# Optimization experiments

Hardware: AMD Instinct MI355X
Metric: run time of the kernel (lower is better)

The kernel has to match this reference:

```python
import jax, jax.numpy as jnp
import numpy as np

B, N, F, W = 8, 2048, 128, 64


def setup_inputs() -> dict:
    key = jax.random.key(0)
    k1, k2, k3, k4 = jax.random.split(key, 4)
    x = jax.random.normal(k1, (B, N, F), dtype=jnp.float32)
    adj = jnp.ones((B, N, N), dtype=bool)  # accepted by forward but unused
    w_key = jax.random.normal(k2, (F, W), dtype=jnp.float32) * 0.1
    w_value = jax.random.normal(k3, (F, F), dtype=jnp.float32) * 0.1
    w_query = jax.random.normal(k4, (F, W), dtype=jnp.float32) * 0.1
    return {"x": x, "adj": adj, "w_key": w_key, "w_value": w_value, "w_query": w_query}


def reference(x, adj, w_key, w_value, w_query):
    # keys/queries: [B, N, W]; values: [B, N, F]
    keys = x @ w_key
    querys = x @ w_query
    values = x @ w_value
    # per-batch softmax(Q K^T) over last dim -> [B, N, N]
    scores = jax.nn.softmax(jnp.einsum('bnw,bmw->bnm', querys, keys), axis=-1)
    # original broadcast-multiply-sum is exactly scores @ values
    out = jnp.einsum('bnm,bmf->bnf', scores, values)
    return out
```

## Files before the change

kernel.cpp:

```cpp
#include <hip/hip_runtime.h>
#include <hip/hip_bf16.h>
#include <math.h>

constexpr int B = 8;
constexpr int N = 2048;
constexpr int F = 128;
constexpr int W = 64;

constexpr int TQ = 64;
constexpr int TK = 64;
constexpr int KSPLIT = 2;
constexpr int TILES_PER_SPLIT = (N / TK) / KSPLIT;

typedef short bf16x8 __attribute__((ext_vector_type(8)));
typedef float f32x4  __attribute__((ext_vector_type(4)));

__device__ inline ushort f2bf(float f) {
  union { float f; uint u; } v; v.f = f;
  uint u = v.u;
  return (ushort)((u + 0x7FFFu + ((u >> 16) & 1u)) >> 16);
}
__device__ inline float bf2f(ushort h) {
  union { uint u; float f; } v; v.u = ((uint)h) << 16;
  return v.f;
}
__device__ inline void splitbf(float f, ushort& hi, ushort& lo) {
  ushort h = f2bf(f);
  hi = h;
  lo = f2bf(f - bf2f(h));
}

__global__ __launch_bounds__(256) void prep_w(
    const float* __restrict__ wq, const float* __restrict__ wk,
    const float* __restrict__ wv, ushort* __restrict__ wth,
    ushort* __restrict__ wtl) {
  int gid = blockIdx.x * 256 + threadIdx.x;
  int n = gid >> 4;
  int k0 = (gid & 15) * 8;
  ushort th[8], tl[8];
#pragma unroll
  for (int j = 0; j < 8; ++j) {
    int k = k0 + j;
    float val = (n < 64)  ? wq[k * W + n]
              : (n < 128) ? wk[k * W + (n - 64)]
                          : wv[k * F + (n - 128)];
    splitbf(val, th[j], tl[j]);
  }
  *(uint4*)&wth[n * 128 + k0] = *(uint4*)th;
  *(uint4*)&wtl[n * 128 + k0] = *(uint4*)tl;
}

__global__ __launch_bounds__(256) void proj_kernel(
    const float* __restrict__ x,
    const ushort* __restrict__ wth, const ushort* __restrict__ wtl,
    ushort* __restrict__ q_h, ushort* __restrict__ q_l,
    ushort* __restrict__ k_h, ushort* __restrict__ k_l,
    ushort* __restrict__ vt_ws) {
  const int tid  = threadIdx.x;
  const int wid  = tid >> 6;
  const int lane = tid & 63;
  const int lg = lane >> 4, li = lane & 15;
  const int rb   = blockIdx.x & 255;
  const int half = blockIdx.x >> 8;
  const int brow0 = rb * 64;
  const int b    = brow0 / N;
  const int nloc = brow0 % N;

  bf16x8 xh[4], xl[4];
  const float* xrow = x + (size_t)(brow0 + wid * 16 + li) * F;
#pragma unroll
  for (int kk = 0; kk < 4; ++kk) {
    float4 a = *(const float4*)&xrow[kk * 32 + lg * 8];
    float4 c = *(const float4*)&xrow[kk * 32 + lg * 8 + 4];
    float vals[8] = {a.x, a.y, a.z, a.w, c.x, c.y, c.z, c.w};
    ushort hh[8], ll[8];
#pragma unroll
    for (int j = 0; j < 8; ++j) splitbf(vals[j], hh[j], ll[j]);
    xh[kk] = *(bf16x8*)hh;
    xl[kk] = *(bf16x8*)ll;
  }

  f32x4 zero = {0.f, 0.f, 0.f, 0.f};
  f32x4 acc[8];
#pragma unroll
  for (int t = 0; t < 8; ++t) acc[t] = zero;

  const ushort* wbh = wth + (size_t)half * 128 * 128;
  const ushort* wbl = wtl + (size_t)half * 128 * 128;

  if (half == 0) {
#pragma unroll
    for (int kk = 0; kk < 4; ++kk)
#pragma unroll
      for (int nt = 0; nt < 8; ++nt) {
        bf16x8 bh = *(const bf16x8*)&wbh[(nt * 16 + li) * 128 + kk * 32 + lg * 8];
        bf16x8 bl = *(const bf16x8*)&wbl[(nt * 16 + li) * 128 + kk * 32 + lg * 8];
        acc[nt] = __builtin_amdgcn_mfma_f32_16x16x32_bf16(xh[kk], bh, acc[nt], 0, 0, 0);
        acc[nt] = __builtin_amdgcn_mfma_f32_16x16x32_bf16(xh[kk], bl, acc[nt], 0, 0, 0);
        acc[nt] = __builtin_amdgcn_mfma_f32_16x16x32_bf16(xl[kk], bh, acc[nt], 0, 0, 0);
      }
#pragma unroll
    for (int nt = 0; nt < 8; ++nt)
#pragma unroll
      for (int r = 0; r < 4; ++r) {
        int row = brow0 + wid * 16 + lg * 4 + r;
        int c = nt * 16 + li;
        ushort hv, lv;
        splitbf(acc[nt][r], hv, lv);
        if (nt < 4) { q_h[row * W + c] = hv;        q_l[row * W + c] = lv; }
        else        { k_h[row * W + (c - 64)] = hv; k_l[row * W + (c - 64)] = lv; }
      }
  } else {
#pragma unroll
    for (int kk = 0; kk < 4; ++kk)
#pragma unroll
      for (int mt = 0; mt < 8; ++mt) {
        bf16x8 ah = *(const bf16x8*)&wbh[(mt * 16 + li) * 128 + kk * 32 + lg * 8];
        bf16x8 al = *(const bf16x8*)&wbl[(mt * 16 + li) * 128 + kk * 32 + lg * 8];
        acc[mt] = __builtin_amdgcn_mfma_f32_16x16x32_bf16(ah, xh[kk], acc[mt], 0, 0, 0);
        acc[mt] = __builtin_amdgcn_mfma_f32_16x16x32_bf16(ah, xl[kk], acc[mt], 0, 0, 0);
        acc[mt] = __builtin_amdgcn_mfma_f32_16x16x32_bf16(al, xh[kk], acc[mt], 0, 0, 0);
      }
#pragma unroll
    for (int mt = 0; mt < 8; ++mt)
#pragma unroll
      for (int r = 0; r < 4; ++r) {
        int f = mt * 16 + lg * 4 + r;
        int n = nloc + wid * 16 + li;
        vt_ws[(size_t)b * F * N + (size_t)f * N + n] = f2bf(acc[mt][r]);
      }
  }
}

constexpr int LP = 72;

__global__ __launch_bounds__(256) void attn_kernel(
    const ushort* __restrict__ q_h, const ushort* __restrict__ q_l,
    const ushort* __restrict__ k_h, const ushort* __restrict__ k_l,
    const ushort* __restrict__ vt_ws,
    float* __restrict__ out,
    float* __restrict__ op1,
    float* __restrict__ lsums) {
  __shared__ ushort ksh[TK][LP];
  __shared__ ushort ksl[TK][LP];
  __shared__ ushort vst[F][LP];
  __shared__ ushort ps[4][16][LP];

  const int tid  = threadIdx.x;
  const int wid  = tid >> 6;
  const int lane = tid & 63;
  const int lg = lane >> 4, li = lane & 15;
  const int b = blockIdx.y, qt = blockIdx.x, split = blockIdx.z;

  const size_t koffb = (size_t)b * N * W;
  const ushort* vb = vt_ws + (size_t)b * F * N;

  const size_t qrow = (size_t)(b * N + qt * TQ + wid * 16 + li) * W;
  bf16x8 qah[2], qal[2];
  qah[0] = *(const bf16x8*)&q_h[qrow + lg * 8];
  qah[1] = *(const bf16x8*)&q_h[qrow + 32 + lg * 8];
  qal[0] = *(const bf16x8*)&q_l[qrow + lg * 8];
  qal[1] = *(const bf16x8*)&q_l[qrow + 32 + lg * 8];

  float l_r[4] = {0.f, 0.f, 0.f, 0.f};
  f32x4 zero = {0.f, 0.f, 0.f, 0.f};
  f32x4 o_acc[8];
#pragma unroll
  for (int t = 0; t < 8; ++t) o_acc[t] = zero;

  const int kt0 = split * TILES_PER_SPLIT;
  for (int kt = kt0; kt < kt0 + TILES_PER_SPLIT; ++kt) {
    __syncthreads();
    const size_t koff = koffb + (size_t)kt * TK * W;
    for (int idx = tid; idx < 512; idx += 256) {
      int row = idx >> 3, c8 = idx & 7;
      *(uint4*)&ksh[row][c8 * 8] = *(const uint4*)&k_h[koff + row * W + c8 * 8];
      *(uint4*)&ksl[row][c8 * 8] = *(const uint4*)&k_l[koff + row * W + c8 * 8];
    }
    for (int idx = tid; idx < 1024; idx += 256) {
      int f = idx >> 3, c8 = idx & 7;
      *(uint4*)&vst[f][c8 * 8] = *(const uint4*)&vb[(size_t)f * N + kt * TK + c8 * 8];
    }
    __syncthreads();

    f32x4 s_acc[4];
#pragma unroll
    for (int nt = 0; nt < 4; ++nt) s_acc[nt] = zero;
#pragma unroll
    for (int kk = 0; kk < 2; ++kk)
#pragma unroll
      for (int nt = 0; nt < 4; ++nt) {
        bf16x8 kh = *(const bf16x8*)&ksh[nt * 16 + li][kk * 32 + lg * 8];
        bf16x8 kl = *(const bf16x8*)&ksl[nt * 16 + li][kk * 32 + lg * 8];
        s_acc[nt] = __builtin_amdgcn_mfma_f32_16x16x32_bf16(qah[kk], kh, s_acc[nt], 0, 0, 0);
        s_acc[nt] = __builtin_amdgcn_mfma_f32_16x16x32_bf16(qah[kk], kl, s_acc[nt], 0, 0, 0);
        s_acc[nt] = __builtin_amdgcn_mfma_f32_16x16x32_bf16(qal[kk], kh, s_acc[nt], 0, 0, 0);
      }

#pragma unroll
    for (int nt = 0; nt < 4; ++nt)
#pragma unroll
      for (int r = 0; r < 4; ++r) {
        float p = __expf(s_acc[nt][r]);
        ushort ph = f2bf(p);
        l_r[r] += bf2f(ph);
        ps[wid][lg * 4 + r][nt * 16 + li] = ph;
      }

#pragma unroll
    for (int kk = 0; kk < 2; ++kk) {
      bf16x8 pa = *(const bf16x8*)&ps[wid][li][kk * 32 + lg * 8];
#pragma unroll
      for (int ft = 0; ft < 8; ++ft) {
        bf16x8 vf = *(const bf16x8*)&vst[ft * 16 + li][kk * 32 + lg * 8];
        o_acc[ft] = __builtin_amdgcn_mfma_f32_16x16x32_bf16(pa, vf, o_acc[ft], 0, 0, 0);
      }
    }
  }

#pragma unroll
  for (int r = 0; r < 4; ++r)
#pragma unroll
    for (int off = 1; off < 16; off <<= 1)
      l_r[r] += __shfl_xor(l_r[r], off, 64);

  float* opb = (split == 0) ? out : op1;
  float* ob = opb + (size_t)(b * N + qt * TQ) * F;
#pragma unroll
  for (int r = 0; r < 4; ++r) {
    int row = wid * 16 + lg * 4 + r;
#pragma unroll
    for (int ft = 0; ft < 8; ++ft)
      ob[row * F + ft * 16 + li] = o_acc[ft][r];
    if (li == 0) {
      size_t gr = (size_t)split * B * N + (size_t)(b * N + qt * TQ) + row;
      lsums[gr] = l_r[r];
    }
  }
}

__global__ __launch_bounds__(256) void combine_kernel(
    const float* __restrict__ op1, const float* __restrict__ lsums,
    float* __restrict__ out) {
  const int gr  = blockIdx.x * 2 + (threadIdx.x >> 7);
  const int col = threadIdx.x & 127;
  const float l0 = lsums[gr];
  const float l1 = lsums[(size_t)B * N + gr];
  const float inv = 1.f / (l0 + l1);
  const size_t idx = (size_t)gr * F + col;
  out[idx] = (out[idx] + op1[idx]) * inv;
}

extern "C" void kernel_launch(void* const* d_in, const int* in_sizes, int n_in,
                              void* d_out, int out_size, void* d_ws, size_t ws_size,
                              hipStream_t stream) {
  const float* x  = (const float*)d_in[0];
  const float* wk = (const float*)d_in[2];
  const float* wv = (const float*)d_in[3];
  const float* wq = (const float*)d_in[4];
  float* out = (float*)d_out;

  constexpr size_t BNW = (size_t)B * N * W;
  ushort* q_h  = (ushort*)d_ws;
  ushort* q_l  = q_h + BNW;
  ushort* k_h  = q_l + BNW;
  ushort* k_l  = k_h + BNW;
  ushort* vt   = k_l + BNW;
  ushort* wth  = vt + (size_t)B * F * N;
  ushort* wtl  = wth + 32768;
  float*  op1  = (float*)(wtl + 32768);
  float*  ls   = op1 + (size_t)B * N * F;

  prep_w<<<16, 256, 0, stream>>>(wq, wk, wv, wth, wtl);
  proj_kernel<<<512, 256, 0, stream>>>(x, wth, wtl, q_h, q_l, k_h, k_l, vt);
  dim3 grid(N / TQ, B, KSPLIT);
  attn_kernel<<<grid, 256, 0, stream>>>(q_h, q_l, k_h, k_l, vt, out, op1, ls);
  combine_kernel<<<B * N / 2, 256, 0, stream>>>(op1, ls, out);
}
```

Baseline: 254.1 us.

## Double query tile to 128 with 512 threads and split keys four ways

```diff
diff --git a/kernel.cpp b/kernel.cpp
--- a/kernel.cpp
+++ b/kernel.cpp
@@ -7,9 +7,9 @@
 constexpr int F = 128;
 constexpr int W = 64;
 
-constexpr int TQ = 64;
+constexpr int TQ = 128;
 constexpr int TK = 64;
-constexpr int KSPLIT = 2;
+constexpr int KSPLIT = 4;
 constexpr int TILES_PER_SPLIT = (N / TK) / KSPLIT;
 
 typedef short bf16x8 __attribute__((ext_vector_type(8)));
@@ -134,17 +134,19 @@
 
 constexpr int LP = 72;
 
-__global__ __launch_bounds__(256) void attn_kernel(
+__global__ __launch_bounds__(512) void attn_kernel(
     const ushort* __restrict__ q_h, const ushort* __restrict__ q_l,
     const ushort* __restrict__ k_h, const ushort* __restrict__ k_l,
     const ushort* __restrict__ vt_ws,
     float* __restrict__ out,
     float* __restrict__ op1,
+    float* __restrict__ op2,
+    float* __restrict__ op3,
     float* __restrict__ lsums) {
   __shared__ ushort ksh[TK][LP];
   __shared__ ushort ksl[TK][LP];
   __shared__ ushort vst[F][LP];
-  __shared__ ushort ps[4][16][LP];
+  __shared__ ushort ps[8][16][LP];
 
   const int tid  = threadIdx.x;
   const int wid  = tid >> 6;
@@ -162,7 +164,7 @@
   qal[0] = *(const bf16x8*)&q_l[qrow + lg * 8];
   qal[1] = *(const bf16x8*)&q_l[qrow + 32 + lg * 8];
 
-  float l_r[4] = {0.f, 0.f, 0.f, 0.f};
+  float l_lane = 0.f;
   f32x4 zero = {0.f, 0.f, 0.f, 0.f};
   f32x4 o_acc[8];
 #pragma unroll
@@ -172,13 +174,14 @@
   for (int kt = kt0; kt < kt0 + TILES_PER_SPLIT; ++kt) {
     __syncthreads();
     const size_t koff = koffb + (size_t)kt * TK * W;
-    for (int idx = tid; idx < 512; idx += 256) {
-      int row = idx >> 3, c8 = idx & 7;
+    {
+      int row = tid >> 3, c8 = tid & 7;
       *(uint4*)&ksh[row][c8 * 8] = *(const uint4*)&k_h[koff + row * W + c8 * 8];
       *(uint4*)&ksl[row][c8 * 8] = *(const uint4*)&k_l[koff + row * W + c8 * 8];
     }
-    for (int idx = tid; idx < 1024; idx += 256) {
-      int f = idx >> 3, c8 = idx & 7;
+#pragma unroll
+    for (int j = 0; j < 2; ++j) {
+      int idx = tid + j * 512, f = idx >> 3, c8 = idx & 7;
       *(uint4*)&vst[f][c8 * 8] = *(const uint4*)&vb[(size_t)f * N + kt * TK + c8 * 8];
     }
     __syncthreads();
@@ -192,9 +195,9 @@
       for (int nt = 0; nt < 4; ++nt) {
         bf16x8 kh = *(const bf16x8*)&ksh[nt * 16 + li][kk * 32 + lg * 8];
         bf16x8 kl = *(const bf16x8*)&ksl[nt * 16 + li][kk * 32 + lg * 8];
-        s_acc[nt] = __builtin_amdgcn_mfma_f32_16x16x32_bf16(qah[kk], kh, s_acc[nt], 0, 0, 0);
-        s_acc[nt] = __builtin_amdgcn_mfma_f32_16x16x32_bf16(qah[kk], kl, s_acc[nt], 0, 0, 0);
-        s_acc[nt] = __builtin_amdgcn_mfma_f32_16x16x32_bf16(qal[kk], kh, s_acc[nt], 0, 0, 0);
+        s_acc[nt] = __builtin_amdgcn_mfma_f32_16x16x32_bf16(kh, qah[kk], s_acc[nt], 0, 0, 0);
+        s_acc[nt] = __builtin_amdgcn_mfma_f32_16x16x32_bf16(kh, qal[kk], s_acc[nt], 0, 0, 0);
+        s_acc[nt] = __builtin_amdgcn_mfma_f32_16x16x32_bf16(kl, qah[kk], s_acc[nt], 0, 0, 0);
       }
 
 #pragma unroll
@@ -203,8 +206,8 @@
       for (int r = 0; r < 4; ++r) {
         float p = __expf(s_acc[nt][r]);
         ushort ph = f2bf(p);
-        l_r[r] += bf2f(ph);
-        ps[wid][lg * 4 + r][nt * 16 + li] = ph;
+        l_lane += bf2f(ph);
+        ps[wid][li][nt * 16 + lg * 4 + r] = ph;
       }
 
 #pragma unroll
@@ -218,13 +221,10 @@
     }
   }
 
-#pragma unroll
-  for (int r = 0; r < 4; ++r)
-#pragma unroll
-    for (int off = 1; off < 16; off <<= 1)
-      l_r[r] += __shfl_xor(l_r[r], off, 64);
-
-  float* opb = (split == 0) ? out : op1;
+  l_lane += __shfl_xor(l_lane, 16, 64);
+  l_lane += __shfl_xor(l_lane, 32, 64);
+
+  float* opb = (split == 0) ? out : (split == 1) ? op1 : (split == 2) ? op2 : op3;
   float* ob = opb + (size_t)(b * N + qt * TQ) * F;
 #pragma unroll
   for (int r = 0; r < 4; ++r) {
@@ -232,23 +232,24 @@
 #pragma unroll
     for (int ft = 0; ft < 8; ++ft)
       ob[row * F + ft * 16 + li] = o_acc[ft][r];
-    if (li == 0) {
-      size_t gr = (size_t)split * B * N + (size_t)(b * N + qt * TQ) + row;
-      lsums[gr] = l_r[r];
-    }
+  }
+  if (lg == 0) {
+    size_t gr = (size_t)split * B * N + (size_t)(b * N + qt * TQ) + wid * 16 + li;
+    lsums[gr] = l_lane;
   }
 }
 
 __global__ __launch_bounds__(256) void combine_kernel(
-    const float* __restrict__ op1, const float* __restrict__ lsums,
+    const float* __restrict__ op1, const float* __restrict__ op2,
+    const float* __restrict__ op3, const float* __restrict__ lsums,
     float* __restrict__ out) {
   const int gr  = blockIdx.x * 2 + (threadIdx.x >> 7);
   const int col = threadIdx.x & 127;
-  const float l0 = lsums[gr];
-  const float l1 = lsums[(size_t)B * N + gr];
-  const float inv = 1.f / (l0 + l1);
+  constexpr size_t BN = (size_t)B * N;
+  const float l = lsums[gr] + lsums[BN + gr] + lsums[2 * BN + gr] + lsums[3 * BN + gr];
+  const float inv = 1.f / l;
   const size_t idx = (size_t)gr * F + col;
-  out[idx] = (out[idx] + op1[idx]) * inv;
+  out[idx] = (out[idx] + op1[idx] + op2[idx] + op3[idx]) * inv;
 }
 
 extern "C" void kernel_launch(void* const* d_in, const int* in_sizes, int n_in,
@@ -261,19 +262,23 @@
   float* out = (float*)d_out;
 
   constexpr size_t BNW = (size_t)B * N * W;
+  constexpr size_t BNF = (size_t)B * N * F;
   ushort* q_h  = (ushort*)d_ws;
   ushort* q_l  = q_h + BNW;
   ushort* k_h  = q_l + BNW;
   ushort* k_l  = k_h + BNW;
   ushort* vt   = k_l + BNW;
-  ushort* wth  = vt + (size_t)B * F * N;
+  ushort* wth  = vt + BNF;
   ushort* wtl  = wth + 32768;
   float*  op1  = (float*)(wtl + 32768);
-  float*  ls   = op1 + (size_t)B * N * F;
+  float*  op2  = op1 + BNF;
+  float*  op3  = op2 + BNF;
+  float*  ls   = op3 + BNF;
 
   prep_w<<<16, 256, 0, stream>>>(wq, wk, wv, wth, wtl);
   proj_kernel<<<512, 256, 0, stream>>>(x, wth, wtl, q_h, q_l, k_h, k_l, vt);
   dim3 grid(N / TQ, B, KSPLIT);
-  attn_kernel<<<grid, 256, 0, stream>>>(q_h, q_l, k_h, k_l, vt, out, op1, ls);
-  combine_kernel<<<B * N / 2, 256, 0, stream>>>(op1, ls, out);
-}
+  attn_kernel<<<grid, 512, 0, stream>>>(q_h, q_l, k_h, k_l, vt,
+                                        out, op1, op2, op3, ls);
+  combine_kernel<<<B * N / 2, 256, 0, stream>>>(op1, op2, op3, ls, out);
+}
```

Measured after the change: 235.1 us. 7.5% less time.
